# Kernel tuning notes

Hardware: AMD Instinct MI355X
Metric: run time of the kernel (lower is better)

## Reference

```python
import math
import jax, jax.numpy as jnp
import numpy as np

B, T, D = 2, 1024, 768          # batch, seq, hidden
H = 12                          # attention heads
DH_ATT = D // H
PH, NK, TOPK, DHK = 4, 256, 32, 128  # pkm heads, num product keys, topk, key dim
DQ = PH * DHK * 2               # pkm query projection width
EPS = 1e-5


def _ln(x, g, b):
    m = jnp.mean(x, -1, keepdims=True)
    v = jnp.var(x, -1, keepdims=True)
    return (x - m) * jax.lax.rsqrt(v + EPS) * g + b


def setup_inputs() -> dict:
    key = jax.random.key(0)
    k = jax.random.split(key, 8)
    n = lambda i, s, sc=0.02: jax.random.normal(k[i], s, jnp.float32) * sc
    z = lambda s: jnp.zeros(s, jnp.float32)
    o = lambda s: jnp.ones(s, jnp.float32)
    return {
        "hidden_states": jax.random.normal(k[0], (B, T, D), jnp.float32),
        "wq": n(1, (D, D)), "bq": z((D,)),
        "wk": n(2, (D, D)), "bk": z((D,)),
        "wv": n(3, (D, D)), "bv": z((D,)),
        "wo": n(4, (D, D)), "bo": z((D,)),
        "ln1_g": o((D,)), "ln1_b": z((D,)),
        "ln2_g": o((D,)), "ln2_b": z((D,)),
        "pkm_wq": n(5, (D, DQ)),
        "bn_g": o((DQ,)), "bn_b": z((DQ,)),
        "pkm_keys": n(6, (PH, NK, 2, DHK), 1.0 / math.sqrt(DHK)),
        "pkm_values": n(7, (NK * NK, D), 1.0 / math.sqrt(D)),
    }


def reference(hidden_states, wq, bq, wk, bk, wv, bv, wo, bo,
              ln1_g, ln1_b, ln2_g, ln2_b,
              pkm_wq, bn_g, bn_b, pkm_keys, pkm_values):
    x = hidden_states
    # ---- pre-norm self-attention + residual ----
    h = _ln(x, ln1_g, ln1_b)
    q = (h @ wq + bq).reshape(B, T, H, DH_ATT)
    k = (h @ wk + bk).reshape(B, T, H, DH_ATT)
    v = (h @ wv + bv).reshape(B, T, H, DH_ATT)
    scores = jnp.einsum('bqhd,bkhd->bhqk', q, k) / math.sqrt(DH_ATT)
    probs = jax.nn.softmax(scores, axis=-1)
    attn_out = jnp.einsum('bhqk,bkhd->bqhd', probs, v).reshape(B, T, D) @ wo + bo
    x = x + attn_out
    # ---- pre-norm PKM + residual ----
    h = _ln(x, ln2_g, ln2_b)
    qf = (h @ pkm_wq).reshape(B * T, DQ)
    # BatchNorm1d over tokens (training-mode batch stats)
    mu = jnp.mean(qf, 0)
    var = jnp.var(qf, 0)
    qn = (qf - mu) * jax.lax.rsqrt(var + EPS) * bn_g + bn_b
    # split into the two sub-key query halves: [2, n, PH, DHK]
    qh = jnp.stack(jnp.split(qn, 2, axis=-1)).reshape(2, B * T, PH, DHK)
    # distances against both sub-key codebooks: [n, PH, 2, NK]
    dots = jnp.einsum('pnhd,hkpd->nhpk', qh, pkm_keys)
    s, idx = jax.lax.top_k(dots, TOPK)                       # [n, PH, 2, TOPK]
    all_s = (s[:, :, 0, :, None] + s[:, :, 1, None, :]).reshape(B * T, PH, TOPK * TOPK)
    all_i = (idx[:, :, 0, :, None] * NK + idx[:, :, 1, None, :]).reshape(B * T, PH, TOPK * TOPK)
    fs, fpos = jax.lax.top_k(all_s, TOPK)                    # [n, PH, TOPK]
    vi = jnp.take_along_axis(all_i, fpos, axis=-1)           # cartesian indices
    attn = jax.nn.softmax(fs, axis=-1)
    # EmbeddingBag(mode='sum') with per_sample_weights: gather + weighted sum over PH*TOPK
    pkm_out = jnp.einsum('nhk,nhkd->nd', attn, pkm_values[vi]).reshape(B, T, D)
    return x + pkm_out
```

## Files before the change

kernel.cpp:

```cpp
#include <hip/hip_runtime.h>
#include <hip/hip_bf16.h>

#define B_  2
#define T_  1024
#define D_  768
#define H_  12
#define NT  2048
#define DQ_ 1024
#define PH_ 4
#define NK_ 256
#define TK_ 32
#define DHK_ 128
#define QKVLD 2304
#define CVHALF 25165824L
#define NKEYS (PH_ * NK_ * 2 * DHK_)
#define PREPBLKS 3584

typedef __attribute__((ext_vector_type(8))) short bf16x8;
typedef __attribute__((ext_vector_type(4))) float f32x4;
typedef __attribute__((ext_vector_type(2))) float f32x2;

static __device__ __forceinline__ unsigned short f2bf(float f) {
    union { float f; unsigned u; } c; c.f = f;
    unsigned r = (c.u + 0x7fffu + ((c.u >> 16) & 1u)) >> 16;
    return (unsigned short)r;
}

static __device__ __forceinline__ float bf2f(unsigned short s) {
    union { unsigned u; float f; } c; c.u = ((unsigned)s) << 16;
    return c.f;
}

__global__ __launch_bounds__(256)
void ln_kernel(const float* __restrict__ x, const float* __restrict__ g,
               const float* __restrict__ b, unsigned short* __restrict__ out,
               int nrows,
               const float* __restrict__ wq, const float* __restrict__ wk,
               const float* __restrict__ wv, const float* __restrict__ wo,
               const float* __restrict__ pwq, const float* __restrict__ keys,
               unsigned short* __restrict__ wqkvT, unsigned short* __restrict__ woT,
               unsigned short* __restrict__ pwqT, unsigned short* __restrict__ keyB) {
    int tid = threadIdx.x;
    if ((int)blockIdx.x >= nrows) {
        int tb = blockIdx.x - nrows;
        if (tb >= 3072) {
            long i = ((long)(tb - 3072) * 256 + tid) * 2;
            if (i + 1 < NKEYS + 1) { keyB[i] = f2bf(keys[i]); keyB[i + 1] = f2bf(keys[i + 1]); }
            return;
        }
        __shared__ float t[32][33];
        const float* W; unsigned short* Wt; int N, kx, ny;
        if (tb < 2304) {
            int z = tb / 576, rem = tb % 576;
            kx = rem % 24; ny = rem / 24; N = 768;
            if (z == 0)      { W = wq; Wt = wqkvT; }
            else if (z == 1) { W = wk; Wt = wqkvT + 589824; }
            else if (z == 2) { W = wv; Wt = wqkvT + 2 * 589824; }
            else             { W = wo; Wt = woT; }
        } else {
            int rem = tb - 2304;
            kx = rem % 24; ny = rem / 24; N = 1024;
            W = pwq; Wt = pwqT;
        }
        int k0 = kx * 32, n0 = ny * 32;
        int tx = tid & 31, ty = tid >> 5;
#pragma unroll
        for (int i = 0; i < 4; ++i)
            t[ty + 8 * i][tx] = W[(long)(k0 + ty + 8 * i) * N + n0 + tx];
        __syncthreads();
#pragma unroll
        for (int i = 0; i < 4; ++i)
            Wt[(long)(n0 + ty + 8 * i) * 768 + k0 + tx] = f2bf(t[tx][ty + 8 * i]);
        return;
    }

    int row = blockIdx.x;
    const float* xr = x + (long)row * D_;
    float v0 = xr[tid], v1 = xr[tid + 256], v2 = xr[tid + 512];
    float s = v0 + v1 + v2, ss = v0 * v0 + v1 * v1 + v2 * v2;
#pragma unroll
    for (int o = 1; o < 64; o <<= 1) { s += __shfl_xor(s, o); ss += __shfl_xor(ss, o); }
    __shared__ float ps[4], pss[4];
    int wid = tid >> 6, lane = tid & 63;
    if (lane == 0) { ps[wid] = s; pss[wid] = ss; }
    __syncthreads();
    s = ps[0] + ps[1] + ps[2] + ps[3];
    ss = pss[0] + pss[1] + pss[2] + pss[3];
    float mean = s * (1.f / D_);
    float var = ss * (1.f / D_) - mean * mean;
    float rs = rsqrtf(var + 1e-5f);
    unsigned short* orow = out + (long)row * D_;
    orow[tid]       = f2bf((v0 - mean) * rs * g[tid]       + b[tid]);
    orow[tid + 256] = f2bf((v1 - mean) * rs * g[tid + 256] + b[tid + 256]);
    orow[tid + 512] = f2bf((v2 - mean) * rs * g[tid + 512] + b[tid + 512]);
}

__global__ __launch_bounds__(256)
void gemm_kernel(const unsigned short* __restrict__ A, int lda,
                 const unsigned short* __restrict__ Bt, int ldb,
                 const float* __restrict__ bias,
                 const float* __restrict__ bias2,
                 const float* __restrict__ bias3,
                 const float* __restrict__ res,
                 float* __restrict__ outF,
                 unsigned short* __restrict__ outB,
                 int ldc, int K, int zmode,
                 const float* __restrict__ cvin,
                 unsigned char* __restrict__ cvout,
                 long cvbase, int cvy0) {
    if (cvin && (int)blockIdx.y >= cvy0) {
        long stride = (long)(gridDim.y - cvy0) * gridDim.x * 256 * 8;
        long idx = cvbase +
            ((long)((blockIdx.y - cvy0) * gridDim.x + blockIdx.x) * 256 + threadIdx.x) * 8;
        long end = cvbase + CVHALF;
#pragma unroll 2
        for (; idx < end; idx += stride) {
            f32x4 a = *(const f32x4*)(cvin + idx);
            f32x4 b = *(const f32x4*)(cvin + idx + 4);
            int lo = __builtin_amdgcn_cvt_pk_fp8_f32(a[0], a[1], 0, false);
            lo = __builtin_amdgcn_cvt_pk_fp8_f32(a[2], a[3], lo, true);
            int hi = __builtin_amdgcn_cvt_pk_fp8_f32(b[0], b[1], 0, false);
            hi = __builtin_amdgcn_cvt_pk_fp8_f32(b[2], b[3], hi, true);
            *(uint2*)(cvout + idx) = make_uint2((unsigned)lo, (unsigned)hi);
        }
        return;
    }
    if (zmode == 1) {
        int z = blockIdx.z, ph = z >> 1, half = z & 1;
        A    += half * 512 + ph * 128;
        Bt   += ph * 65536 + half * 128;
        if (outF) outF += ph * 512 + half * 256;
        if (outB) outB += ph * 512 + half * 256;
    }
    const int tid = threadIdx.x;
    const int w = tid >> 6, lane = tid & 63;
    const int ls = lane & 15, g = lane >> 4;
    const int m0 = blockIdx.x * 64, n0 = blockIdx.y * 64;

    __shared__ unsigned short As[64][40];
    __shared__ unsigned short Bs[64][40];

    f32x4 acc[4];
#pragma unroll
    for (int c = 0; c < 4; ++c) acc[c] = (f32x4){0.f, 0.f, 0.f, 0.f};

    const int lrow = tid >> 2, lseg = tid & 3;
    const unsigned short* gA = A + (long)(m0 + lrow) * lda + lseg * 8;
    const unsigned short* gB = Bt + (long)(n0 + lrow) * ldb + lseg * 8;

    for (int kt = 0; kt < K; kt += 32) {
        __syncthreads();
        *(int4*)&As[lrow][lseg * 8] = *(const int4*)(gA + kt);
        *(int4*)&Bs[lrow][lseg * 8] = *(const int4*)(gB + kt);
        __syncthreads();
        bf16x8 bfr = *(const bf16x8*)&Bs[w * 16 + ls][g * 8];
#pragma unroll
        for (int c = 0; c < 4; ++c) {
            bf16x8 afr = *(const bf16x8*)&As[c * 16 + ls][g * 8];
            acc[c] = __builtin_amdgcn_mfma_f32_16x16x32_bf16(afr, bfr, acc[c], 0, 0, 0);
        }
    }
#pragma unroll
    for (int c = 0; c < 4; ++c) {
#pragma unroll
        for (int r = 0; r < 4; ++r) {
            int row = m0 + c * 16 + g * 4 + r;
            int col = n0 + w * 16 + ls;
            float v = acc[c][r];
            if (bias) {
                const float* bp = bias; int cc = col;
                if (zmode == 2) {
                    int sel = col >= 1536 ? 2 : (col >= 768 ? 1 : 0);
                    bp = sel == 0 ? bias : (sel == 1 ? bias2 : bias3);
                    cc = col - sel * 768;
                }
                v += bp[cc];
            }
            long off = (long)row * ldc + col;
            if (res)  v += res[off];
            if (outF) outF[off] = v;
            if (outB) outB[off] = f2bf(v);
        }
    }
}

__global__ __launch_bounds__(256)
void attn_mfma_kernel(const unsigned short* __restrict__ qkv,
                      unsigned short* __restrict__ outg) {
    int bh = blockIdx.x, bb = bh / H_, hh = bh % H_;
    int q0 = blockIdx.y * 64;
    int tid = threadIdx.x, wv = tid >> 6, lane = tid & 63;
    int ls = lane & 15, g = lane >> 4;

    __shared__ unsigned short Klds[128 * 64];
    __shared__ unsigned short Vlds[64 * 128];
    __shared__ unsigned short Plds[4][16 * 128];

    const unsigned short* qrow = qkv + (long)(bb * T_ + q0 + wv * 16 + ls) * QKVLD + hh * 64 + g * 8;
    bf16x8 qf0 = *(const bf16x8*)qrow;
    bf16x8 qf1 = *(const bf16x8*)(qrow + 32);

    f32x4 o_acc[4];
#pragma unroll
    for (int nf = 0; nf < 4; ++nf) o_acc[nf] = (f32x4){0.f, 0.f, 0.f, 0.f};
    float mrun[4] = {-1e30f, -1e30f, -1e30f, -1e30f};
    float lrun[4] = {0.f, 0.f, 0.f, 0.f};

    char* pbase = (char*)&Plds[wv][0];
    const int d0 = (tid & 7) * 8, kvq = tid >> 3;

    bf16x8 kreg[4], vreg[4];
    auto loadKV = [&](int kvb) {
#pragma unroll
        for (int i = 0; i < 4; ++i) {
            int c = tid + i * 256;
            kreg[i] = *(const bf16x8*)(qkv + (long)(bb * T_ + kvb + (c >> 3)) * QKVLD + 768 + hh * 64 + (c & 7) * 8);
        }
        const unsigned short* vb = qkv + (long)(bb * T_ + kvb + kvq * 4) * QKVLD + 1536 + hh * 64 + d0;
#pragma unroll
        for (int i = 0; i < 4; ++i) vreg[i] = *(const bf16x8*)(vb + i * QKVLD);
    };

    loadKV(0);
    for (int kt = 0; kt < T_ / 128; ++kt) {
        __syncthreads();
#pragma unroll
        for (int i = 0; i < 4; ++i) {
            int c = tid + i * 256;
            int kv = c >> 3, dc = c & 7;
            *(bf16x8*)((char*)Klds + ((kv * 128 + dc * 16) ^ ((kv & 7) << 4))) = kreg[i];
        }
#pragma unroll
        for (int j = 0; j < 8; ++j) {
            unsigned lo = (unsigned)(unsigned short)vreg[0][j] | ((unsigned)(unsigned short)vreg[1][j] << 16);
            unsigned hi = (unsigned)(unsigned short)vreg[2][j] | ((unsigned)(unsigned short)vreg[3][j] << 16);
            int d = d0 + j;
            *(uint2*)((char*)Vlds + ((d * 256 + kvq * 8) ^ ((d & 7) << 4))) = make_uint2(lo, hi);
        }
        __syncthreads();
        if (kt + 1 < T_ / 128) loadKV((kt + 1) * 128);

        f32x4 sa[8];
#pragma unroll
        for (int f = 0; f < 8; ++f) sa[f] = (f32x4){0.f, 0.f, 0.f, 0.f};
        __builtin_amdgcn_s_setprio(1);
#pragma unroll
        for (int f = 0; f < 8; ++f) {
            int kv = f * 16 + ls;
            bf16x8 b0 = *(const bf16x8*)((char*)Klds + ((kv * 128 + g * 16) ^ ((kv & 7) << 4)));
            bf16x8 b1 = *(const bf16x8*)((char*)Klds + ((kv * 128 + 64 + g * 16) ^ ((kv & 7) << 4)));
            sa[f] = __builtin_amdgcn_mfma_f32_16x16x32_bf16(qf0, b0, sa[f], 0, 0, 0);
            sa[f] = __builtin_amdgcn_mfma_f32_16x16x32_bf16(qf1, b1, sa[f], 0, 0, 0);
        }
        __builtin_amdgcn_s_setprio(0);

        float pw[8][4];
#pragma unroll
        for (int f = 0; f < 8; ++f)
#pragma unroll
            for (int r = 0; r < 4; ++r) pw[f][r] = sa[f][r] * 0.125f;
#pragma unroll
        for (int r = 0; r < 4; ++r) {
            float m = pw[0][r];
#pragma unroll
            for (int f = 1; f < 8; ++f) m = fmaxf(m, pw[f][r]);
            m = fmaxf(m, __shfl_xor(m, 1));
            m = fmaxf(m, __shfl_xor(m, 2));
            m = fmaxf(m, __shfl_xor(m, 4));
            m = fmaxf(m, __shfl_xor(m, 8));
            if (m > mrun[r] + 8.f) {
                float fac = __expf(mrun[r] - m);
                lrun[r] *= fac;
#pragma unroll
                for (int nf = 0; nf < 4; ++nf) o_acc[nf][r] *= fac;
                mrun[r] = m;
            }
            float s = 0.f;
#pragma unroll
            for (int f = 0; f < 8; ++f) { float e = __expf(pw[f][r] - mrun[r]); pw[f][r] = e; s += e; }
            s += __shfl_xor(s, 1); s += __shfl_xor(s, 2);
            s += __shfl_xor(s, 4); s += __shfl_xor(s, 8);
            lrun[r] += s;
        }

#pragma unroll
        for (int f = 0; f < 8; ++f)
#pragma unroll
            for (int r = 0; r < 4; ++r) {
                int qr = g * 4 + r, col = ls + 16 * f;
                *(unsigned short*)(pbase + ((qr * 256 + col * 2) ^ ((qr & 7) << 4))) = f2bf(pw[f][r]);
            }

        __builtin_amdgcn_s_setprio(1);
#pragma unroll
        for (int ks = 0; ks < 4; ++ks) {
            bf16x8 pa = *(const bf16x8*)(pbase + ((ls * 256 + ks * 64 + g * 16) ^ ((ls & 7) << 4)));
#pragma unroll
            for (int nf = 0; nf < 4; ++nf) {
                int d = nf * 16 + ls;
                bf16x8 bv = *(const bf16x8*)((char*)Vlds + ((d * 256 + ks * 64 + g * 16) ^ ((d & 7) << 4)));
                o_acc[nf] = __builtin_amdgcn_mfma_f32_16x16x32_bf16(pa, bv, o_acc[nf], 0, 0, 0);
            }
        }
        __builtin_amdgcn_s_setprio(0);
    }

    float inv[4];
#pragma unroll
    for (int r = 0; r < 4; ++r) inv[r] = 1.f / lrun[r];
#pragma unroll
    for (int nf = 0; nf < 4; ++nf)
#pragma unroll
        for (int r = 0; r < 4; ++r) {
            long row = bb * T_ + q0 + wv * 16 + g * 4 + r;
            outg[row * D_ + hh * 64 + nf * 16 + ls] = f2bf(o_acc[nf][r] * inv[r]);
        }
}

__global__ __launch_bounds__(256)
void bn_part(const float* __restrict__ qf, float* __restrict__ pS, float* __restrict__ pSS) {
    int c = blockIdx.y * 256 + threadIdx.x;
    int r0 = blockIdx.x * 32;
    float s = 0.f, ss = 0.f;
#pragma unroll 4
    for (int r = 0; r < 32; ++r) {
        float v = qf[(long)(r0 + r) * DQ_ + c];
        s += v; ss += v * v;
    }
    pS[(long)blockIdx.x * DQ_ + c] = s;
    pSS[(long)blockIdx.x * DQ_ + c] = ss;
}

__global__ __launch_bounds__(256)
void qnf_kernel(const float* __restrict__ qf, const float* __restrict__ pS,
                const float* __restrict__ pSS, const float* __restrict__ g,
                const float* __restrict__ b, unsigned short* __restrict__ qn) {
    int c = blockIdx.y * 256 + threadIdx.x;
    float s = 0.f, ss = 0.f;
#pragma unroll 8
    for (int i = 0; i < 64; ++i) { s += pS[(long)i * DQ_ + c]; ss += pSS[(long)i * DQ_ + c]; }
    float m = s * (1.f / NT);
    float rs = rsqrtf(ss * (1.f / NT) - m * m + 1e-5f);
    float gg = g[c] * rs;
    float bb = b[c] - m * gg;
    int r0 = blockIdx.x * 32;
#pragma unroll 4
    for (int r = 0; r < 32; ++r) {
        long o = (long)(r0 + r) * DQ_ + c;
        qn[o] = f2bf(qf[o] * gg + bb);
    }
}

__global__ __launch_bounds__(256)
void topk_kernel(const unsigned short* __restrict__ dots, float* __restrict__ fs, int* __restrict__ vi) {
    static const unsigned short tab[128] = {
        0,1,2,3,4,5,6,7,8,9,10,11,12,13,14,15,16,17,18,19,20,21,22,23,24,25,26,27,28,29,30,31,
        32,33,34,35,36,37,38,39,40,41,42,43,44,45,46,47,
        64,65,66,67,68,69,70,71,72,73,
        96,97,98,99,100,101,102,103,
        128,129,130,131,132,133,
        160,161,162,163,164,
        192,193,194,195,
        224,225,226,227,
        256,257,258,
        288,289,290,
        320,321, 352,353, 384,385, 416,417, 448,449, 480,481,
        512,544,576,608,640,672,704,736,768,800,832,864,896,928,960,992,
        0xFFFF,0xFFFF,0xFFFF,0xFFFF,0xFFFF,0xFFFF,0xFFFF,0xFFFF,0xFFFF
    };
    __shared__ float sv[2][64];
    __shared__ int   sidx[2][64];
    int tid = threadIdx.x, wv = tid >> 6, lane = tid & 63;
    int slot = wv >> 1, half = wv & 1;
    long task = (long)blockIdx.x * 2 + slot;
    const unsigned short* d = dots + (task >> 2) * 2048 + (task & 3) * 512 + half * 256;

    float v0 = bf2f(d[lane]), v1 = bf2f(d[lane + 64]);
    float v2 = bf2f(d[lane + 128]), v3 = bf2f(d[lane + 192]);
#pragma unroll 1
    for (int t = 0; t < 32; ++t) {
        float bm = v0; int ba = 0;
        if (v1 > bm) { bm = v1; ba = 1; }
        if (v2 > bm) { bm = v2; ba = 2; }
        if (v3 > bm) { bm = v3; ba = 3; }
        float wm = bm;
#pragma unroll
        for (int o = 32; o >= 1; o >>= 1) wm = fmaxf(wm, __shfl_xor(wm, o));
        unsigned long long msk = __ballot(bm == wm);
        int owner = (int)__builtin_ctzll(msk);
        if (lane == owner) {
            sv[slot][half * 32 + t] = wm;
            sidx[slot][half * 32 + t] = ba * 64 + lane;
            if (ba == 0) v0 = -1e30f;
            else if (ba == 1) v1 = -1e30f;
            else if (ba == 2) v2 = -1e30f;
            else v3 = -1e30f;
        }
    }
    __syncthreads();
    if (half) return;

    unsigned short t0 = tab[lane], t1 = tab[lane + 64];
    float c0 = -1e30f, c1 = -1e30f;
    int id0 = 0, id1 = 0;
    {
        int i = t0 >> 5, j = t0 & 31;
        c0 = sv[slot][i] + sv[slot][32 + j];
        id0 = sidx[slot][i] * NK_ + sidx[slot][32 + j];
    }
    if (t1 != 0xFFFF) {
        int i = t1 >> 5, j = t1 & 31;
        c1 = sv[slot][i] + sv[slot][32 + j];
        id1 = sidx[slot][i] * NK_ + sidx[slot][32 + j];
    }

    float* fo = fs + task * 32;
    int*   vo = vi + task * 32;
#pragma unroll 1
    for (int t = 0; t < 32; ++t) {
        float bm = c0; int sel = 0;
        if (c1 > bm) { bm = c1; sel = 1; }
        float wm = bm;
#pragma unroll
        for (int o = 32; o >= 1; o >>= 1) wm = fmaxf(wm, __shfl_xor(wm, o));
        unsigned long long msk = __ballot(bm == wm);
        int owner = (int)__builtin_ctzll(msk);
        if (lane == owner) {
            fo[t] = wm;
            vo[t] = sel ? id1 : id0;
            if (sel) c1 = -1e30f; else c0 = -1e30f;
        }
    }
}

__global__ __launch_bounds__(384)
void pkm_out_fp8(const float* __restrict__ fs, const int* __restrict__ vi,
                 const unsigned char* __restrict__ vals8, const float* __restrict__ x1,
                 float* __restrict__ outp) {
    int n = blockIdx.x, tid = threadIdx.x;
    __shared__ float w[128];
    __shared__ int   rows[128];
    __shared__ float red[3 * 768];
    if (tid < 128) {
        float e = fs[(long)n * 128 + tid];
        rows[tid] = vi[(long)n * 128 + tid];
        float m = e;
#pragma unroll
        for (int o = 16; o >= 1; o >>= 1) m = fmaxf(m, __shfl_xor(m, o));
        float ex = __expf(e - m);
        float s = ex;
#pragma unroll
        for (int o = 16; o >= 1; o >>= 1) s += __shfl_xor(s, o);
        w[tid] = ex / s;
    }
    __syncthreads();
    int slot = tid / 96, chunk = tid % 96;
    float a0=0.f,a1=0.f,a2=0.f,a3=0.f,a4=0.f,a5=0.f,a6=0.f,a7=0.f;
#pragma unroll 4
    for (int e = 0; e < 32; ++e) {
        int er = e * 4 + slot;
        float wgt = w[er];
        long ro = (long)rows[er] * D_;
        uint2 v = *(const uint2*)(vals8 + ro + chunk * 8);
        f32x2 f0 = __builtin_amdgcn_cvt_pk_f32_fp8((int)v.x, false);
        f32x2 f1 = __builtin_amdgcn_cvt_pk_f32_fp8((int)v.x, true);
        f32x2 f2 = __builtin_amdgcn_cvt_pk_f32_fp8((int)v.y, false);
        f32x2 f3 = __builtin_amdgcn_cvt_pk_f32_fp8((int)v.y, true);
        a0 += wgt * f0[0]; a1 += wgt * f0[1]; a2 += wgt * f1[0]; a3 += wgt * f1[1];
        a4 += wgt * f2[0]; a5 += wgt * f2[1]; a6 += wgt * f3[0]; a7 += wgt * f3[1];
    }
    if (slot > 0) {
        float* rp = &red[(slot - 1) * 768 + chunk * 8];
        rp[0]=a0; rp[1]=a1; rp[2]=a2; rp[3]=a3; rp[4]=a4; rp[5]=a5; rp[6]=a6; rp[7]=a7;
    }
    __syncthreads();
    if (slot == 0) {
        long o = (long)n * D_ + chunk * 8;
        const float* r0 = &red[chunk * 8];
        const float* r1 = &red[768 + chunk * 8];
        const float* r2 = &red[1536 + chunk * 8];
        f32x4 xa = *(const f32x4*)(x1 + o);
        f32x4 xb = *(const f32x4*)(x1 + o + 4);
        f32x4 o1 = { a0 + r0[0] + r1[0] + r2[0] + xa[0], a1 + r0[1] + r1[1] + r2[1] + xa[1],
                     a2 + r0[2] + r1[2] + r2[2] + xa[2], a3 + r0[3] + r1[3] + r2[3] + xa[3] };
        f32x4 o2 = { a4 + r0[4] + r1[4] + r2[4] + xb[0], a5 + r0[5] + r1[5] + r2[5] + xb[1],
                     a6 + r0[6] + r1[6] + r2[6] + xb[2], a7 + r0[7] + r1[7] + r2[7] + xb[3] };
        *(f32x4*)(outp + o) = o1;
        *(f32x4*)(outp + o + 4) = o2;
    }
}

__global__ __launch_bounds__(384)
void pkm_out_f32(const float* __restrict__ fs, const int* __restrict__ vi,
                 const float* __restrict__ values, const float* __restrict__ x1,
                 float* __restrict__ outp) {
    int n = blockIdx.x, tid = threadIdx.x;
    __shared__ float w[128];
    __shared__ int   rows[128];
    __shared__ float red[768];
    if (tid < 128) {
        float e = fs[(long)n * 128 + tid];
        rows[tid] = vi[(long)n * 128 + tid];
        float m = e;
#pragma unroll
        for (int o = 16; o >= 1; o >>= 1) m = fmaxf(m, __shfl_xor(m, o));
        float ex = __expf(e - m);
        float s = ex;
#pragma unroll
        for (int o = 16; o >= 1; o >>= 1) s += __shfl_xor(s, o);
        w[tid] = ex / s;
    }
    __syncthreads();
    int slot = tid / 192, chunk = tid % 192;
    float a0 = 0.f, a1 = 0.f, a2 = 0.f, a3 = 0.f;
#pragma unroll 4
    for (int e = 0; e < 64; ++e) {
        int er = e * 2 + slot;
        float wgt = w[er];
        long ro = (long)rows[er] * D_;
        f32x4 v = *(const f32x4*)(values + ro + chunk * 4);
        a0 += wgt * v[0]; a1 += wgt * v[1]; a2 += wgt * v[2]; a3 += wgt * v[3];
    }
    if (slot == 1) {
        f32x4 t = {a0, a1, a2, a3};
        *(f32x4*)&red[chunk * 4] = t;
    }
    __syncthreads();
    if (slot == 0) {
        f32x4 o = *(const f32x4*)&red[chunk * 4];
        f32x4 xr = *(const f32x4*)(x1 + (long)n * D_ + chunk * 4);
        o[0] += a0 + xr[0]; o[1] += a1 + xr[1]; o[2] += a2 + xr[2]; o[3] += a3 + xr[3];
        *(f32x4*)(outp + (long)n * D_ + chunk * 4) = o;
    }
}

extern "C" void kernel_launch(void* const* d_in, const int* in_sizes, int n_in,
                              void* d_out, int out_size, void* d_ws, size_t ws_size,
                              hipStream_t stream) {
    const float* x    = (const float*)d_in[0];
    const float* wq   = (const float*)d_in[1];
    const float* bq   = (const float*)d_in[2];
    const float* wk   = (const float*)d_in[3];
    const float* bk   = (const float*)d_in[4];
    const float* wv   = (const float*)d_in[5];
    const float* bv   = (const float*)d_in[6];
    const float* wo   = (const float*)d_in[7];
    const float* bo   = (const float*)d_in[8];
    const float* ln1g = (const float*)d_in[9];
    const float* ln1b = (const float*)d_in[10];
    const float* ln2g = (const float*)d_in[11];
    const float* ln2b = (const float*)d_in[12];
    const float* pwq  = (const float*)d_in[13];
    const float* bng  = (const float*)d_in[14];
    const float* bnb  = (const float*)d_in[15];
    const float* keys = (const float*)d_in[16];
    const float* vals = (const float*)d_in[17];
    float* out = (float*)d_out;

    char* p = (char*)d_ws;
    auto alloc = [&](size_t bytes) -> char* {
        char* r = p; p += (bytes + 255) & ~(size_t)255; return r;
    };
    unsigned short* wqkvT = (unsigned short*)alloc((size_t)3 * D_ * D_ * 2);
    unsigned short* woT   = (unsigned short*)alloc((size_t)D_ * D_ * 2);
    unsigned short* pwqT  = (unsigned short*)alloc((size_t)D_ * DQ_ * 2);
    unsigned short* keyB  = (unsigned short*)alloc((size_t)NKEYS * 2);
    unsigned short* h1    = (unsigned short*)alloc((size_t)NT * D_ * 2);
    unsigned short* qkvB  = (unsigned short*)alloc((size_t)NT * QKVLD * 2);
    unsigned short* aout  = (unsigned short*)alloc((size_t)NT * D_ * 2);
    float* x1             = (float*)alloc((size_t)NT * D_ * 4);
    unsigned short* h2    = (unsigned short*)alloc((size_t)NT * D_ * 2);
    float* qf             = (float*)alloc((size_t)NT * DQ_ * 4);
    float* pS             = (float*)alloc((size_t)64 * DQ_ * 4);
    float* pSS            = (float*)alloc((size_t)64 * DQ_ * 4);
    unsigned short* qnB   = (unsigned short*)alloc((size_t)NT * DQ_ * 2);
    unsigned short* dots  = (unsigned short*)alloc((size_t)NT * 2048 * 2);
    float* fsb            = (float*)alloc((size_t)NT * PH_ * 32 * 4);
    int*   vib            = (int*)alloc((size_t)NT * PH_ * 32 * 4);

    size_t used = (size_t)(p - (char*)d_ws);
    size_t vbytes = (size_t)NK_ * NK_ * D_;
    bool useTab = (used + vbytes + 256) <= ws_size;
    unsigned char* vals8 = nullptr;
    if (useTab) vals8 = (unsigned char*)alloc(vbytes);

    ln_kernel<<<NT + PREPBLKS, 256, 0, stream>>>(
        x, ln1g, ln1b, h1, NT, wq, wk, wv, wo, pwq, keys, wqkvT, woT, pwqT, keyB);
    gemm_kernel<<<dim3(32, useTab ? 52 : 36), 256, 0, stream>>>(
        h1, D_, wqkvT, D_, bq, bk, bv, nullptr, nullptr, qkvB, QKVLD, D_, 2,
        useTab ? vals : nullptr, vals8, 0L, 36);
    attn_mfma_kernel<<<dim3(B_ * H_, T_ / 64), 256, 0, stream>>>(qkvB, aout);
    gemm_kernel<<<dim3(32, 12), 256, 0, stream>>>(
        aout, D_, woT, D_, bo, nullptr, nullptr, x, x1, nullptr, D_, D_, 0,
        nullptr, nullptr, 0L, 0);
    ln_kernel<<<NT, 256, 0, stream>>>(
        x1, ln2g, ln2b, h2, NT, nullptr, nullptr, nullptr, nullptr, nullptr, nullptr,
        nullptr, nullptr, nullptr, nullptr);
    gemm_kernel<<<dim3(32, useTab ? 32 : 16), 256, 0, stream>>>(
        h2, D_, pwqT, D_, nullptr, nullptr, nullptr, nullptr, qf, nullptr, DQ_, D_, 0,
        useTab ? vals : nullptr, vals8, CVHALF, 16);
    bn_part<<<dim3(64, 4), 256, 0, stream>>>(qf, pS, pSS);
    qnf_kernel<<<dim3(64, 4), 256, 0, stream>>>(qf, pS, pSS, bng, bnb, qnB);
    gemm_kernel<<<dim3(32, 4, 8), 256, 0, stream>>>(
        qnB, DQ_, keyB, 256, nullptr, nullptr, nullptr, nullptr, nullptr, dots, 2048, DHK_, 1,
        nullptr, nullptr, 0L, 0);
    topk_kernel<<<(NT * PH_) / 2, 256, 0, stream>>>(dots, fsb, vib);
    if (useTab)
        pkm_out_fp8<<<NT, 384, 0, stream>>>(fsb, vib, vals8, x1, out);
    else
        pkm_out_f32<<<NT, 384, 0, stream>>>(fsb, vib, vals, x1, out);
}
```

Measured before the change: 264.1 us.

## Double attention query tile per block and store PKM query projection in bf16

Result: no change. 259.2 us (-1.9%).

```diff
diff --git a/kernel.cpp b/kernel.cpp
--- a/kernel.cpp
+++ b/kernel.cpp
@@ -184,17 +184,17 @@
     }
 }
 
-__global__ __launch_bounds__(256)
+__global__ __launch_bounds__(512)
 void attn_mfma_kernel(const unsigned short* __restrict__ qkv,
                       unsigned short* __restrict__ outg) {
     int bh = blockIdx.x, bb = bh / H_, hh = bh % H_;
-    int q0 = blockIdx.y * 64;
+    int q0 = blockIdx.y * 128;
     int tid = threadIdx.x, wv = tid >> 6, lane = tid & 63;
     int ls = lane & 15, g = lane >> 4;
 
     __shared__ unsigned short Klds[128 * 64];
     __shared__ unsigned short Vlds[64 * 128];
-    __shared__ unsigned short Plds[4][16 * 128];
+    __shared__ unsigned short Plds[8][16 * 128];
 
     const unsigned short* qrow = qkv + (long)(bb * T_ + q0 + wv * 16 + ls) * QKVLD + hh * 64 + g * 8;
     bf16x8 qf0 = *(const bf16x8*)qrow;
@@ -207,35 +207,43 @@
     float lrun[4] = {0.f, 0.f, 0.f, 0.f};
 
     char* pbase = (char*)&Plds[wv][0];
-    const int d0 = (tid & 7) * 8, kvq = tid >> 3;
-
-    bf16x8 kreg[4], vreg[4];
+    const bool doK = tid < 256;
+    const int t2 = tid & 255;
+    const int d0 = (t2 & 7) * 8, kvq = t2 >> 3;
+
+    bf16x8 streg[4];
     auto loadKV = [&](int kvb) {
-#pragma unroll
-        for (int i = 0; i < 4; ++i) {
-            int c = tid + i * 256;
-            kreg[i] = *(const bf16x8*)(qkv + (long)(bb * T_ + kvb + (c >> 3)) * QKVLD + 768 + hh * 64 + (c & 7) * 8);
-        }
-        const unsigned short* vb = qkv + (long)(bb * T_ + kvb + kvq * 4) * QKVLD + 1536 + hh * 64 + d0;
-#pragma unroll
-        for (int i = 0; i < 4; ++i) vreg[i] = *(const bf16x8*)(vb + i * QKVLD);
+        if (doK) {
+#pragma unroll
+            for (int i = 0; i < 4; ++i) {
+                int c = t2 + i * 256;
+                streg[i] = *(const bf16x8*)(qkv + (long)(bb * T_ + kvb + (c >> 3)) * QKVLD + 768 + hh * 64 + (c & 7) * 8);
+            }
+        } else {
+            const unsigned short* vb = qkv + (long)(bb * T_ + kvb + kvq * 4) * QKVLD + 1536 + hh * 64 + d0;
+#pragma unroll
+            for (int i = 0; i < 4; ++i) streg[i] = *(const bf16x8*)(vb + i * QKVLD);
+        }
     };
 
     loadKV(0);
     for (int kt = 0; kt < T_ / 128; ++kt) {
         __syncthreads();
-#pragma unroll
-        for (int i = 0; i < 4; ++i) {
-            int c = tid + i * 256;
-            int kv = c >> 3, dc = c & 7;
-            *(bf16x8*)((char*)Klds + ((kv * 128 + dc * 16) ^ ((kv & 7) << 4))) = kreg[i];
-        }
-#pragma unroll
-        for (int j = 0; j < 8; ++j) {
-            unsigned lo = (unsigned)(unsigned short)vreg[0][j] | ((unsigned)(unsigned short)vreg[1][j] << 16);
-            unsigned hi = (unsigned)(unsigned short)vreg[2][j] | ((unsigned)(unsigned short)vreg[3][j] << 16);
-            int d = d0 + j;
-            *(uint2*)((char*)Vlds + ((d * 256 + kvq * 8) ^ ((d & 7) << 4))) = make_uint2(lo, hi);
+        if (doK) {
+#pragma unroll
+            for (int i = 0; i < 4; ++i) {
+                int c = t2 + i * 256;
+                int kv = c >> 3, dc = c & 7;
+                *(bf16x8*)((char*)Klds + ((kv * 128 + dc * 16) ^ ((kv & 7) << 4))) = streg[i];
+            }
+        } else {
+#pragma unroll
+            for (int j = 0; j < 8; ++j) {
+                unsigned lo = (unsigned)(unsigned short)streg[0][j] | ((unsigned)(unsigned short)streg[1][j] << 16);
+                unsigned hi = (unsigned)(unsigned short)streg[2][j] | ((unsigned)(unsigned short)streg[3][j] << 16);
+                int d = d0 + j;
+                *(uint2*)((char*)Vlds + ((d * 256 + kvq * 8) ^ ((d & 7) << 4))) = make_uint2(lo, hi);
+            }
         }
         __syncthreads();
         if (kt + 1 < T_ / 128) loadKV((kt + 1) * 128);
@@ -318,13 +326,13 @@
 }
 
 __global__ __launch_bounds__(256)
-void bn_part(const float* __restrict__ qf, float* __restrict__ pS, float* __restrict__ pSS) {
+void bn_part(const unsigned short* __restrict__ qf, float* __restrict__ pS, float* __restrict__ pSS) {
     int c = blockIdx.y * 256 + threadIdx.x;
     int r0 = blockIdx.x * 32;
     float s = 0.f, ss = 0.f;
 #pragma unroll 4
     for (int r = 0; r < 32; ++r) {
-        float v = qf[(long)(r0 + r) * DQ_ + c];
+        float v = bf2f(qf[(long)(r0 + r) * DQ_ + c]);
         s += v; ss += v * v;
     }
     pS[(long)blockIdx.x * DQ_ + c] = s;
@@ -332,7 +340,7 @@
 }
 
 __global__ __launch_bounds__(256)
-void qnf_kernel(const float* __restrict__ qf, const float* __restrict__ pS,
+void qnf_kernel(const unsigned short* __restrict__ qf, const float* __restrict__ pS,
                 const float* __restrict__ pSS, const float* __restrict__ g,
                 const float* __restrict__ b, unsigned short* __restrict__ qn) {
     int c = blockIdx.y * 256 + threadIdx.x;
@@ -347,7 +355,7 @@
 #pragma unroll 4
     for (int r = 0; r < 32; ++r) {
         long o = (long)(r0 + r) * DQ_ + c;
-        qn[o] = f2bf(qf[o] * gg + bb);
+        qn[o] = f2bf(bf2f(qf[o]) * gg + bb);
     }
 }
 
@@ -570,7 +578,7 @@
     unsigned short* aout  = (unsigned short*)alloc((size_t)NT * D_ * 2);
     float* x1             = (float*)alloc((size_t)NT * D_ * 4);
     unsigned short* h2    = (unsigned short*)alloc((size_t)NT * D_ * 2);
-    float* qf             = (float*)alloc((size_t)NT * DQ_ * 4);
+    unsigned short* qfB   = (unsigned short*)alloc((size_t)NT * DQ_ * 2);
     float* pS             = (float*)alloc((size_t)64 * DQ_ * 4);
     float* pSS            = (float*)alloc((size_t)64 * DQ_ * 4);
     unsigned short* qnB   = (unsigned short*)alloc((size_t)NT * DQ_ * 2);
@@ -589,7 +597,7 @@
     gemm_kernel<<<dim3(32, useTab ? 52 : 36), 256, 0, stream>>>(
         h1, D_, wqkvT, D_, bq, bk, bv, nullptr, nullptr, qkvB, QKVLD, D_, 2,
         useTab ? vals : nullptr, vals8, 0L, 36);
-    attn_mfma_kernel<<<dim3(B_ * H_, T_ / 64), 256, 0, stream>>>(qkvB, aout);
+    attn_mfma_kernel<<<dim3(B_ * H_, T_ / 128), 512, 0, stream>>>(qkvB, aout);
     gemm_kernel<<<dim3(32, 12), 256, 0, stream>>>(
         aout, D_, woT, D_, bo, nullptr, nullptr, x, x1, nullptr, D_, D_, 0,
         nullptr, nullptr, 0L, 0);
@@ -597,10 +605,10 @@
         x1, ln2g, ln2b, h2, NT, nullptr, nullptr, nullptr, nullptr, nullptr, nullptr,
         nullptr, nullptr, nullptr, nullptr);
     gemm_kernel<<<dim3(32, useTab ? 32 : 16), 256, 0, stream>>>(
-        h2, D_, pwqT, D_, nullptr, nullptr, nullptr, nullptr, qf, nullptr, DQ_, D_, 0,
+        h2, D_, pwqT, D_, nullptr, nullptr, nullptr, nullptr, nullptr, qfB, DQ_, D_, 0,
         useTab ? vals : nullptr, vals8, CVHALF, 16);
-    bn_part<<<dim3(64, 4), 256, 0, stream>>>(qf, pS, pSS);
-    qnf_kernel<<<dim3(64, 4), 256, 0, stream>>>(qf, pS, pSS, bng, bnb, qnB);
+    bn_part<<<dim3(64, 4), 256, 0, stream>>>(qfB, pS, pSS);
+    qnf_kernel<<<dim3(64, 4), 256, 0, stream>>>(qfB, pS, pSS, bng, bnb, qnB);
     gemm_kernel<<<dim3(32, 4, 8), 256, 0, stream>>>(
         qnB, DQ_, keyB, 256, nullptr, nullptr, nullptr, nullptr, nullptr, dots, 2048, DHK_, 1,
         nullptr, nullptr, 0L, 0);
```
